# Kernel optimization log

Measured on AMD Instinct MI355X. Metric: run time of the kernel, lower is better.

## Reference

```python
import jax, jax.numpy as jnp
import numpy as np

IN_CH = 128
OUT_CH = 128
INPUT_LEN = 512
KERNEL = 8
STRIDE = 1
OUT_LEN = (INPUT_LEN - KERNEL) // STRIDE + 1  # 505
BATCH = 64


def setup_inputs() -> dict:
    key = jax.random.key(0)
    kx, kw, kb = jax.random.split(key, 3)
    x = jax.random.normal(kx, (BATCH, IN_CH, INPUT_LEN), dtype=jnp.float32)
    weight = jax.random.normal(kw, (OUT_LEN, OUT_CH, IN_CH, KERNEL), dtype=jnp.float32)
    bias = jax.random.normal(kb, (OUT_CH, OUT_LEN), dtype=jnp.float32)
    return {"x": x, "weight": weight, "bias": bias}


def reference(x, weight, bias):
    # unfold: gather sliding windows -> [b, i, l_out, k]
    idx = jnp.arange(OUT_LEN)[:, None] * STRIDE + jnp.arange(KERNEL)[None, :]  # [l, k]
    x_unf = x[:, :, idx]  # [b, i, l, k]
    # per-position independent GEMM: 'blik,loik->bol' with x permuted to bilk
    out = jnp.einsum('bilk,loik->bol', x_unf, weight)
    out = out + bias[None, :, :]
    return out
```

## Files before the change

### kernel.cpp

```cpp
#include <hip/hip_runtime.h>
#include <hip/hip_bf16.h>

#define BATCH 64
#define IN_CH 128
#define ILEN  512
#define OLEN  505
#define OCH   128
#define KDIM  1024
#define BK    64
#define NCHK  16
#define NWG   OLEN

typedef float  f32x4  __attribute__((ext_vector_type(4)));
typedef short  bf16x8 __attribute__((ext_vector_type(8)));
typedef unsigned short u16x8 __attribute__((ext_vector_type(8)));
typedef u16x8 u16x8a __attribute__((aligned(4)));

__device__ __forceinline__ unsigned short f2bf(float f) {
  union { __hip_bfloat16 h; unsigned short s; } u;
  u.h = __float2bfloat16(f);
  return u.s;
}

__global__ __launch_bounds__(256) void lc1d_cvt(const float* __restrict__ x,
                                                unsigned short* __restrict__ xbe,
                                                unsigned short* __restrict__ xbo) {
  const int gid = blockIdx.x * 256 + threadIdx.x;
  const int row = gid >> 6;
  const int t8  = (gid & 63) << 3;
  const float* src = x + (size_t)row * ILEN + t8;
  const f32x4 v0 = *reinterpret_cast<const f32x4*>(src);
  const f32x4 v1 = *reinterpret_cast<const f32x4*>(src + 4);
  const float e8 = (t8 + 8 < ILEN) ? src[8] : 0.f;
  u16x8 e, o;
#pragma unroll
  for (int j = 0; j < 4; ++j) { e[j] = f2bf(v0[j]); e[4 + j] = f2bf(v1[j]); }
  o[0] = e[1]; o[1] = e[2]; o[2] = e[3];
  o[3] = e[4]; o[4] = e[5]; o[5] = e[6]; o[6] = e[7];
  o[7] = f2bf(e8);
  *reinterpret_cast<u16x8*>(xbe + (size_t)row * ILEN + t8) = e;
  *reinterpret_cast<u16x8*>(xbo + (size_t)row * ILEN + t8) = o;
}

template <bool USE_TMP>
__global__ __launch_bounds__(256, 2) void lc1d_main(
    const unsigned short* __restrict__ xbe, const unsigned short* __restrict__ xbo,
    const float* __restrict__ w, const float* __restrict__ bias,
    float* __restrict__ outp) {
  const int orig = blockIdx.x;
  const int xcd = orig & 7, idx = orig >> 3;
  const int q = NWG / 8, rm = NWG % 8;
  const int l = (xcd < rm ? xcd * (q + 1) : rm * (q + 1) + (xcd - rm) * q) + idx;

  const int tid  = threadIdx.x;
  const int lane = tid & 63;
  const int wn   = tid >> 6;
  const int r    = lane & 15;
  const int h    = lane >> 4;

  __shared__ float Bs[2][2][BK * 64];
  __shared__ short As[2][BATCH * 64];

  f32x4 acc[2][4];
#pragma unroll
  for (int oh = 0; oh < 2; ++oh)
#pragma unroll
    for (int m = 0; m < 4; ++m) acc[oh][m] = (f32x4){0.f, 0.f, 0.f, 0.f};

  const float* __restrict__ wl = w + (size_t)l * (OCH * KDIM);
  const unsigned short* __restrict__ xw =
      ((l & 1) ? xbo : xbe) + (size_t)(l & ~1);

  const int so  = tid >> 4;
  const int sc  = tid & 15;
  const int ssw = ((so & 7) << 1) | ((so >> 3) & 1);
  const int bA = tid & 63;
  const int iw = tid >> 6;

  u16x8 va, vb;
  auto loadA2 = [&](int kc) {
    const int i0 = kc * 8 + iw * 2;
    const unsigned short* p = xw + (size_t)(bA * IN_CH + i0) * ILEN;
    va = *reinterpret_cast<const u16x8a*>(p);
    vb = *reinterpret_cast<const u16x8a*>(p + ILEN);
  };
  auto writeA2 = [&](int buf) {
    const int c0 = iw * 2;
    *reinterpret_cast<u16x8*>(&As[buf][bA * 64 + ((c0 ^ (bA & 7)) << 3)]) = va;
    *reinterpret_cast<u16x8*>(&As[buf][bA * 64 + (((c0 + 1) ^ (bA & 7)) << 3)]) = vb;
  };
  auto stageB = [&](int buf, int kc, int oh) {
    const float* wo = wl + (size_t)oh * 64 * KDIM;
#pragma unroll
    for (int it = 0; it < 4; ++it) {
      const int ob = it * 16 + so;
      const float* src = wo + (size_t)ob * KDIM + kc * BK + (sc ^ ssw) * 4;
      __builtin_amdgcn_global_load_lds(
          (const __attribute__((address_space(1))) void*)src,
          (__attribute__((address_space(3))) void*)&Bs[buf][oh][ob * 64 + sc * 4],
          16, 0, 0);
    }
  };

  const int rsw = ((r & 7) << 1) | ((r >> 3) & 1);
  auto compute = [&](int cur, int oh) {
    const int ob = wn * 16 + r;
#pragma unroll
    for (int ks = 0; ks < 2; ++ks) {
      const int c0 = ks * 8 + h * 2;
      const f32x4 blo = *reinterpret_cast<const f32x4*>(
          &Bs[cur][oh][ob * 64 + ((c0) ^ rsw) * 4]);
      const f32x4 bhi = *reinterpret_cast<const f32x4*>(
          &Bs[cur][oh][ob * 64 + ((c0 + 1) ^ rsw) * 4]);
      bf16x8 bfr;
#pragma unroll
      for (int j = 0; j < 4; ++j) {
        bfr[j]     = (short)f2bf(blo[j]);
        bfr[4 + j] = (short)f2bf(bhi[j]);
      }
#pragma unroll
      for (int mt = 0; mt < 4; ++mt) {
        const int b = mt * 16 + r;
        const bf16x8 afr = *reinterpret_cast<const bf16x8*>(
            &As[cur][b * 64 + (((ks * 4 + h) ^ (r & 7)) << 3)]);
        acc[oh][mt] =
            __builtin_amdgcn_mfma_f32_16x16x32_bf16(afr, bfr, acc[oh][mt], 0, 0, 0);
      }
    }
  };

  loadA2(0);
  stageB(0, 0, 0);
  stageB(0, 0, 1);
  writeA2(0);
  asm volatile("s_waitcnt vmcnt(0) lgkmcnt(0)" ::: "memory");
  __builtin_amdgcn_sched_barrier(0);
  __builtin_amdgcn_s_barrier();
  __builtin_amdgcn_sched_barrier(0);

  for (int kc = 0; kc < NCHK; ++kc) {
    const int cur = kc & 1, nxt = cur ^ 1;
    if (kc + 1 < NCHK) {
      loadA2(kc + 1);
      stageB(nxt, kc + 1, 0);
      stageB(nxt, kc + 1, 1);
    }
    __builtin_amdgcn_sched_barrier(0);
    compute(cur, 0);
    compute(cur, 1);
    if (kc + 1 < NCHK) {
      writeA2(nxt);
      asm volatile("s_waitcnt vmcnt(0) lgkmcnt(0)" ::: "memory");
      __builtin_amdgcn_sched_barrier(0);
      __builtin_amdgcn_s_barrier();
      __builtin_amdgcn_sched_barrier(0);
    }
  }

#pragma unroll
  for (int oh = 0; oh < 2; ++oh) {
    const int og = oh * 64 + wn * 16 + r;
    if (USE_TMP) {
      float* t = outp + (size_t)l * (BATCH * OCH) + og;
#pragma unroll
      for (int mt = 0; mt < 4; ++mt)
#pragma unroll
        for (int j = 0; j < 4; ++j) {
          const int b = mt * 16 + h * 4 + j;
          t[(size_t)b * OCH] = acc[oh][mt][j];
        }
    } else {
      const float bv = bias[og * OLEN + l];
#pragma unroll
      for (int mt = 0; mt < 4; ++mt)
#pragma unroll
        for (int j = 0; j < 4; ++j) {
          const int b = mt * 16 + h * 4 + j;
          outp[(size_t)b * (OCH * OLEN) + (size_t)og * OLEN + l] = acc[oh][mt][j] + bv;
        }
    }
  }
}

__global__ __launch_bounds__(256) void lc1d_tr(const float* __restrict__ tmp,
                                               const float* __restrict__ bias,
                                               float* __restrict__ out) {
  const int l0  = blockIdx.x * 64;
  const int bo0 = blockIdx.y * 64;
  const int tid = threadIdx.x;
  __shared__ float t[64][65];

  const int boj = tid & 63, lq = tid >> 6;
#pragma unroll
  for (int rr = 0; rr < 16; ++rr) {
    const int li = rr * 4 + lq;
    const int l  = l0 + li;
    if (l < OLEN) t[li][boj] = tmp[(size_t)l * (BATCH * OCH) + bo0 + boj];
  }
  __syncthreads();
  const int lj = tid & 63, bq = tid >> 6;
  const int l  = l0 + lj;
#pragma unroll
  for (int rr = 0; rr < 16; ++rr) {
    const int bl = rr * 4 + bq;
    const int bo = bo0 + bl;
    if (l < OLEN) {
      const int oc = bo & (OCH - 1);
      out[(size_t)bo * OLEN + l] = t[lj][bl] + bias[oc * OLEN + l];
    }
  }
}

__global__ void lc1d_naive(const float* __restrict__ x, const float* __restrict__ w,
                           const float* __restrict__ bias, float* __restrict__ out) {
  const int l = blockIdx.x, o = blockIdx.y, b = threadIdx.x;
  const float* wr = w + ((size_t)l * OCH + o) * KDIM;
  const float* xr = x + (size_t)b * (IN_CH * ILEN);
  float s = 0.f;
  for (int i = 0; i < IN_CH; ++i)
#pragma unroll
    for (int k = 0; k < 8; ++k) s += xr[i * ILEN + l + k] * wr[i * 8 + k];
  out[((size_t)b * OCH + o) * OLEN + l] = s + bias[o * OLEN + l];
}

extern "C" void kernel_launch(void* const* d_in, const int* in_sizes, int n_in,
                              void* d_out, int out_size, void* d_ws, size_t ws_size,
                              hipStream_t stream) {
  const float* x    = (const float*)d_in[0];
  const float* w    = (const float*)d_in[1];
  const float* bias = (const float*)d_in[2];
  float* out        = (float*)d_out;

  const size_t TMPB = (size_t)OLEN * BATCH * OCH * sizeof(float);
  const size_t off1 = (TMPB + 255) & ~(size_t)255;
  const size_t XBB  = (size_t)BATCH * IN_CH * ILEN * sizeof(short);
  const size_t need = off1 + 2 * XBB;

  if (ws_size >= need) {
    float* tmp = (float*)d_ws;
    unsigned short* xbe = (unsigned short*)((char*)d_ws + off1);
    unsigned short* xbo = (unsigned short*)((char*)d_ws + off1 + XBB);
    lc1d_cvt<<<dim3(2048), 256, 0, stream>>>(x, xbe, xbo);
    lc1d_main<true><<<dim3(NWG), 256, 0, stream>>>(xbe, xbo, w, bias, tmp);
    lc1d_tr<<<dim3(8, 128), 256, 0, stream>>>(tmp, bias, out);
  } else {
    lc1d_naive<<<dim3(OLEN, OCH), BATCH, 0, stream>>>(x, w, bias, out);
  }
}
```

Before: 105.8 us.

## Load A fragments directly from global into registers, drop A LDS staging

Removes the shared-memory staging buffer for the activation (A) operand. Each lane now loads its MFMA A fragments straight from global memory into double-buffered registers, prefetching the next chunk while the current one computes. The wait now keeps the 8 in-flight A loads outstanding (vmcnt(8)) so only the B LDS loads must finish before the barrier. This cuts LDS writes and reads for A and frees LDS, at the cost of more registers, a fully unrolled k-loop, and less-coalesced global loads that each wave issues redundantly.

```diff
diff --git a/kernel.cpp b/kernel.cpp
--- a/kernel.cpp
+++ b/kernel.cpp
@@ -59,7 +59,6 @@
   const int h    = lane >> 4;
 
   __shared__ float Bs[2][2][BK * 64];
-  __shared__ short As[2][BATCH * 64];
 
   f32x4 acc[2][4];
 #pragma unroll
@@ -74,21 +73,7 @@
   const int so  = tid >> 4;
   const int sc  = tid & 15;
   const int ssw = ((so & 7) << 1) | ((so >> 3) & 1);
-  const int bA = tid & 63;
-  const int iw = tid >> 6;
-
-  u16x8 va, vb;
-  auto loadA2 = [&](int kc) {
-    const int i0 = kc * 8 + iw * 2;
-    const unsigned short* p = xw + (size_t)(bA * IN_CH + i0) * ILEN;
-    va = *reinterpret_cast<const u16x8a*>(p);
-    vb = *reinterpret_cast<const u16x8a*>(p + ILEN);
-  };
-  auto writeA2 = [&](int buf) {
-    const int c0 = iw * 2;
-    *reinterpret_cast<u16x8*>(&As[buf][bA * 64 + ((c0 ^ (bA & 7)) << 3)]) = va;
-    *reinterpret_cast<u16x8*>(&As[buf][bA * 64 + (((c0 + 1) ^ (bA & 7)) << 3)]) = vb;
-  };
+
   auto stageB = [&](int buf, int kc, int oh) {
     const float* wo = wl + (size_t)oh * 64 * KDIM;
 #pragma unroll
@@ -102,8 +87,22 @@
     }
   };
 
+  u16x8 paE[4][2], paO[4][2];
+  const unsigned short* __restrict__ xbase =
+      xw + (size_t)(r * IN_CH + h) * ILEN;
+
+  auto prefA = [&](u16x8 (&pa)[4][2], int kc) {
+#pragma unroll
+    for (int mt = 0; mt < 4; ++mt) {
+      const unsigned short* p =
+          xbase + (size_t)(mt * 16 * IN_CH + kc * 8) * ILEN;
+      pa[mt][0] = *reinterpret_cast<const u16x8a*>(p);
+      pa[mt][1] = *reinterpret_cast<const u16x8a*>(p + 4 * ILEN);
+    }
+  };
+
   const int rsw = ((r & 7) << 1) | ((r >> 3) & 1);
-  auto compute = [&](int cur, int oh) {
+  auto compute = [&](int cur, u16x8 (&pa)[4][2], int oh) {
     const int ob = wn * 16 + r;
 #pragma unroll
     for (int ks = 0; ks < 2; ++ks) {
@@ -120,37 +119,34 @@
       }
 #pragma unroll
       for (int mt = 0; mt < 4; ++mt) {
-        const int b = mt * 16 + r;
-        const bf16x8 afr = *reinterpret_cast<const bf16x8*>(
-            &As[cur][b * 64 + (((ks * 4 + h) ^ (r & 7)) << 3)]);
+        const bf16x8 afr = (bf16x8)pa[mt][ks];
         acc[oh][mt] =
             __builtin_amdgcn_mfma_f32_16x16x32_bf16(afr, bfr, acc[oh][mt], 0, 0, 0);
       }
     }
   };
 
-  loadA2(0);
   stageB(0, 0, 0);
   stageB(0, 0, 1);
-  writeA2(0);
-  asm volatile("s_waitcnt vmcnt(0) lgkmcnt(0)" ::: "memory");
+  prefA(paE, 0);
+  asm volatile("s_waitcnt vmcnt(8)" ::: "memory");
   __builtin_amdgcn_sched_barrier(0);
   __builtin_amdgcn_s_barrier();
   __builtin_amdgcn_sched_barrier(0);
 
+#pragma unroll
   for (int kc = 0; kc < NCHK; ++kc) {
     const int cur = kc & 1, nxt = cur ^ 1;
     if (kc + 1 < NCHK) {
-      loadA2(kc + 1);
       stageB(nxt, kc + 1, 0);
       stageB(nxt, kc + 1, 1);
+      if ((kc & 1) == 0) prefA(paO, kc + 1); else prefA(paE, kc + 1);
     }
     __builtin_amdgcn_sched_barrier(0);
-    compute(cur, 0);
-    compute(cur, 1);
+    if ((kc & 1) == 0) { compute(cur, paE, 0); compute(cur, paE, 1); }
+    else               { compute(cur, paO, 0); compute(cur, paO, 1); }
     if (kc + 1 < NCHK) {
-      writeA2(nxt);
-      asm volatile("s_waitcnt vmcnt(0) lgkmcnt(0)" ::: "memory");
+      asm volatile("s_waitcnt vmcnt(8) lgkmcnt(0)" ::: "memory");
       __builtin_amdgcn_sched_barrier(0);
       __builtin_amdgcn_s_barrier();
       __builtin_amdgcn_sched_barrier(0);
```

Measured after the change: 149.7 us. 41.5% more time.

## Stage weights through registers as bf16 with two-chunk-ahead prefetch

Applied to the files above, without the earlier changes.

Weights are now loaded from global memory into registers two K-chunks ahead, converted to bf16 once, and written to LDS as bf16. The old path used direct global-to-LDS fp32 loads and converted inside compute. This halves LDS footprint for B and removes per-wave redundant conversions, enabling 3 workgroups per CU via launch bounds. The cost is higher register pressure (two sets of 8 f32x4 prefetch buffers) and a fully unrolled K loop, which may cause spills under the tighter occupancy bound.

```diff
diff --git a/kernel.cpp b/kernel.cpp
--- a/kernel.cpp
+++ b/kernel.cpp
@@ -43,7 +43,7 @@
 }
 
 template <bool USE_TMP>
-__global__ __launch_bounds__(256, 2) void lc1d_main(
+__global__ __launch_bounds__(256, 3) void lc1d_main(
     const unsigned short* __restrict__ xbe, const unsigned short* __restrict__ xbo,
     const float* __restrict__ w, const float* __restrict__ bias,
     float* __restrict__ outp) {
@@ -58,8 +58,8 @@
   const int r    = lane & 15;
   const int h    = lane >> 4;
 
-  __shared__ float Bs[2][2][BK * 64];
-  __shared__ short As[2][BATCH * 64];
+  __shared__ short Bs[2][OCH * BK];
+  __shared__ short As[2][BATCH * BK];
 
   f32x4 acc[2][4];
 #pragma unroll
@@ -71,86 +71,88 @@
   const unsigned short* __restrict__ xw =
       ((l & 1) ? xbo : xbe) + (size_t)(l & ~1);
 
-  const int so  = tid >> 4;
-  const int sc  = tid & 15;
-  const int ssw = ((so & 7) << 1) | ((so >> 3) & 1);
   const int bA = tid & 63;
   const int iw = tid >> 6;
-
   u16x8 va, vb;
-  auto loadA2 = [&](int kc) {
-    const int i0 = kc * 8 + iw * 2;
-    const unsigned short* p = xw + (size_t)(bA * IN_CH + i0) * ILEN;
+  auto loadA = [&](int kc) {
+    const unsigned short* p = xw + (size_t)(bA * IN_CH + kc * 8 + iw * 2) * ILEN;
     va = *reinterpret_cast<const u16x8a*>(p);
     vb = *reinterpret_cast<const u16x8a*>(p + ILEN);
   };
-  auto writeA2 = [&](int buf) {
+  auto writeA = [&](int buf) {
     const int c0 = iw * 2;
     *reinterpret_cast<u16x8*>(&As[buf][bA * 64 + ((c0 ^ (bA & 7)) << 3)]) = va;
     *reinterpret_cast<u16x8*>(&As[buf][bA * 64 + (((c0 + 1) ^ (bA & 7)) << 3)]) = vb;
   };
-  auto stageB = [&](int buf, int kc, int oh) {
-    const float* wo = wl + (size_t)oh * 64 * KDIM;
+
+  const int sc3 = tid & 7;
+  const int soB = tid >> 3;
+  f32x4 bb0[4][2], bb1[4][2];
+  auto loadB = [&](f32x4 (&bb)[4][2], int kc) {
 #pragma unroll
     for (int it = 0; it < 4; ++it) {
-      const int ob = it * 16 + so;
-      const float* src = wo + (size_t)ob * KDIM + kc * BK + (sc ^ ssw) * 4;
-      __builtin_amdgcn_global_load_lds(
-          (const __attribute__((address_space(1))) void*)src,
-          (__attribute__((address_space(3))) void*)&Bs[buf][oh][ob * 64 + sc * 4],
-          16, 0, 0);
-    }
-  };
-
-  const int rsw = ((r & 7) << 1) | ((r >> 3) & 1);
+      const int o = it * 32 + soB;
+      const float* src = wl + (size_t)o * KDIM + kc * BK + sc3 * 8;
+      bb[it][0] = *reinterpret_cast<const f32x4*>(src);
+      bb[it][1] = *reinterpret_cast<const f32x4*>(src + 4);
+    }
+  };
+  auto writeB = [&](const f32x4 (&bb)[4][2], int buf) {
+#pragma unroll
+    for (int it = 0; it < 4; ++it) {
+      const int o = it * 32 + soB;
+      u16x8 v;
+#pragma unroll
+      for (int j = 0; j < 4; ++j) {
+        v[j]     = f2bf(bb[it][0][j]);
+        v[4 + j] = f2bf(bb[it][1][j]);
+      }
+      *reinterpret_cast<u16x8*>(&Bs[buf][o * 64 + ((sc3 ^ (o & 7)) << 3)]) = v;
+    }
+  };
+
   auto compute = [&](int cur, int oh) {
-    const int ob = wn * 16 + r;
+    const int ob = oh * 64 + wn * 16 + r;
 #pragma unroll
     for (int ks = 0; ks < 2; ++ks) {
-      const int c0 = ks * 8 + h * 2;
-      const f32x4 blo = *reinterpret_cast<const f32x4*>(
-          &Bs[cur][oh][ob * 64 + ((c0) ^ rsw) * 4]);
-      const f32x4 bhi = *reinterpret_cast<const f32x4*>(
-          &Bs[cur][oh][ob * 64 + ((c0 + 1) ^ rsw) * 4]);
-      bf16x8 bfr;
-#pragma unroll
-      for (int j = 0; j < 4; ++j) {
-        bfr[j]     = (short)f2bf(blo[j]);
-        bfr[4 + j] = (short)f2bf(bhi[j]);
-      }
+      const int c = ks * 4 + h;
+      const bf16x8 bfr = *reinterpret_cast<const bf16x8*>(
+          &Bs[cur][ob * 64 + ((c ^ (ob & 7)) << 3)]);
 #pragma unroll
       for (int mt = 0; mt < 4; ++mt) {
         const int b = mt * 16 + r;
         const bf16x8 afr = *reinterpret_cast<const bf16x8*>(
-            &As[cur][b * 64 + (((ks * 4 + h) ^ (r & 7)) << 3)]);
+            &As[cur][b * 64 + ((c ^ (b & 7)) << 3)]);
         acc[oh][mt] =
             __builtin_amdgcn_mfma_f32_16x16x32_bf16(afr, bfr, acc[oh][mt], 0, 0, 0);
       }
     }
   };
 
-  loadA2(0);
-  stageB(0, 0, 0);
-  stageB(0, 0, 1);
-  writeA2(0);
-  asm volatile("s_waitcnt vmcnt(0) lgkmcnt(0)" ::: "memory");
+  loadA(0);
+  loadB(bb0, 0);
+  loadB(bb1, 1);
+  writeA(0);
+  writeB(bb0, 0);
+  asm volatile("s_waitcnt lgkmcnt(0)" ::: "memory");
   __builtin_amdgcn_sched_barrier(0);
   __builtin_amdgcn_s_barrier();
   __builtin_amdgcn_sched_barrier(0);
 
+#pragma unroll
   for (int kc = 0; kc < NCHK; ++kc) {
     const int cur = kc & 1, nxt = cur ^ 1;
-    if (kc + 1 < NCHK) {
-      loadA2(kc + 1);
-      stageB(nxt, kc + 1, 0);
-      stageB(nxt, kc + 1, 1);
+    if (kc + 1 < NCHK) loadA(kc + 1);
+    if (kc + 2 < NCHK) {
+      if ((kc & 1) == 0) loadB(bb0, kc + 2); else loadB(bb1, kc + 2);
     }
     __builtin_amdgcn_sched_barrier(0);
     compute(cur, 0);
     compute(cur, 1);
     if (kc + 1 < NCHK) {
-      writeA2(nxt);
-      asm volatile("s_waitcnt vmcnt(0) lgkmcnt(0)" ::: "memory");
+      writeA(nxt);
+      if ((kc & 1) == 0) writeB(bb1, nxt); else writeB(bb0, nxt);
+      asm volatile("s_waitcnt lgkmcnt(0)" ::: "memory");
       __builtin_amdgcn_sched_barrier(0);
       __builtin_amdgcn_s_barrier();
       __builtin_amdgcn_sched_barrier(0);
```

After: 113.1 us. 1.07x slower.

## Split output-channel halves across workgroups, prefetch A two chunks ahead, store bf16 temp

Applied to the files above, without the earlier changes.

Launches one workgroup per (position, output-channel half), which doubles the grid and halves LDS and accumulator use so three workgroups can fit per CU. A-operand global loads now run two chunks ahead using alternating register sets and a partial vmcnt wait, which is meant to hide global latency behind compute. The intermediate buffer is written as bf16 instead of fp32 to cut temp write and read traffic, at the cost of extra rounding error in the output. Each workgroup now reads the shared input tile separately, so input reads are duplicated.

```diff
diff --git a/kernel.cpp b/kernel.cpp
--- a/kernel.cpp
+++ b/kernel.cpp
@@ -9,17 +9,23 @@
 #define KDIM  1024
 #define BK    64
 #define NCHK  16
-#define NWG   OLEN
+#define NWG   (OLEN * 2)
 
 typedef float  f32x4  __attribute__((ext_vector_type(4)));
 typedef short  bf16x8 __attribute__((ext_vector_type(8)));
 typedef unsigned short u16x8 __attribute__((ext_vector_type(8)));
 typedef u16x8 u16x8a __attribute__((aligned(4)));
 
-__device__ __forceinline__ unsigned short f2bf(float f) {
+__device__ __forceinline__ unsigned short f2bfu(float f) {
   union { __hip_bfloat16 h; unsigned short s; } u;
   u.h = __float2bfloat16(f);
   return u.s;
+}
+__device__ __forceinline__ short f2bf(float f) { return (short)f2bfu(f); }
+__device__ __forceinline__ float bf2f(unsigned short s) {
+  union { unsigned int u; float f; } u;
+  u.u = ((unsigned int)s) << 16;
+  return u.f;
 }
 
 __global__ __launch_bounds__(256) void lc1d_cvt(const float* __restrict__ x,
@@ -34,23 +40,25 @@
   const float e8 = (t8 + 8 < ILEN) ? src[8] : 0.f;
   u16x8 e, o;
 #pragma unroll
-  for (int j = 0; j < 4; ++j) { e[j] = f2bf(v0[j]); e[4 + j] = f2bf(v1[j]); }
+  for (int j = 0; j < 4; ++j) { e[j] = f2bfu(v0[j]); e[4 + j] = f2bfu(v1[j]); }
   o[0] = e[1]; o[1] = e[2]; o[2] = e[3];
   o[3] = e[4]; o[4] = e[5]; o[5] = e[6]; o[6] = e[7];
-  o[7] = f2bf(e8);
+  o[7] = f2bfu(e8);
   *reinterpret_cast<u16x8*>(xbe + (size_t)row * ILEN + t8) = e;
   *reinterpret_cast<u16x8*>(xbo + (size_t)row * ILEN + t8) = o;
 }
 
 template <bool USE_TMP>
-__global__ __launch_bounds__(256, 2) void lc1d_main(
+__global__ __launch_bounds__(256, 3) void lc1d_main(
     const unsigned short* __restrict__ xbe, const unsigned short* __restrict__ xbo,
     const float* __restrict__ w, const float* __restrict__ bias,
-    float* __restrict__ outp) {
+    void* __restrict__ outp) {
   const int orig = blockIdx.x;
   const int xcd = orig & 7, idx = orig >> 3;
   const int q = NWG / 8, rm = NWG % 8;
-  const int l = (xcd < rm ? xcd * (q + 1) : rm * (q + 1) + (xcd - rm) * q) + idx;
+  const int wg = (xcd < rm ? xcd * (q + 1) : rm * (q + 1) + (xcd - rm) * q) + idx;
+  const int l  = wg >> 1;
+  const int oh = wg & 1;
 
   const int tid  = threadIdx.x;
   const int lane = tid & 63;
@@ -58,131 +66,132 @@
   const int r    = lane & 15;
   const int h    = lane >> 4;
 
-  __shared__ float Bs[2][2][BK * 64];
+  __shared__ float Bs[2][BK * 64];
   __shared__ short As[2][BATCH * 64];
 
-  f32x4 acc[2][4];
-#pragma unroll
-  for (int oh = 0; oh < 2; ++oh)
-#pragma unroll
-    for (int m = 0; m < 4; ++m) acc[oh][m] = (f32x4){0.f, 0.f, 0.f, 0.f};
-
-  const float* __restrict__ wl = w + (size_t)l * (OCH * KDIM);
+  f32x4 acc[4];
+#pragma unroll
+  for (int m = 0; m < 4; ++m) acc[m] = (f32x4){0.f, 0.f, 0.f, 0.f};
+
+  const float* __restrict__ wo =
+      w + (size_t)l * (OCH * KDIM) + (size_t)oh * 64 * KDIM;
   const unsigned short* __restrict__ xw =
       ((l & 1) ? xbo : xbe) + (size_t)(l & ~1);
 
   const int so  = tid >> 4;
   const int sc  = tid & 15;
   const int ssw = ((so & 7) << 1) | ((so >> 3) & 1);
-  const int bA = tid & 63;
-  const int iw = tid >> 6;
-
-  u16x8 va, vb;
-  auto loadA2 = [&](int kc) {
-    const int i0 = kc * 8 + iw * 2;
-    const unsigned short* p = xw + (size_t)(bA * IN_CH + i0) * ILEN;
-    va = *reinterpret_cast<const u16x8a*>(p);
-    vb = *reinterpret_cast<const u16x8a*>(p + ILEN);
-  };
-  auto writeA2 = [&](int buf) {
-    const int c0 = iw * 2;
-    *reinterpret_cast<u16x8*>(&As[buf][bA * 64 + ((c0 ^ (bA & 7)) << 3)]) = va;
-    *reinterpret_cast<u16x8*>(&As[buf][bA * 64 + (((c0 + 1) ^ (bA & 7)) << 3)]) = vb;
-  };
-  auto stageB = [&](int buf, int kc, int oh) {
-    const float* wo = wl + (size_t)oh * 64 * KDIM;
+  auto stageB = [&](int buf, int kc) {
 #pragma unroll
     for (int it = 0; it < 4; ++it) {
       const int ob = it * 16 + so;
       const float* src = wo + (size_t)ob * KDIM + kc * BK + (sc ^ ssw) * 4;
       __builtin_amdgcn_global_load_lds(
           (const __attribute__((address_space(1))) void*)src,
-          (__attribute__((address_space(3))) void*)&Bs[buf][oh][ob * 64 + sc * 4],
+          (__attribute__((address_space(3))) void*)&Bs[buf][ob * 64 + sc * 4],
           16, 0, 0);
     }
   };
 
+  const int bA = tid & 63;
+  const int iw = tid >> 6;
+  u16x8 vaE, vbE, vaO, vbO;
+  auto loadA2 = [&](u16x8& va, u16x8& vb, int kc) {
+    const unsigned short* p = xw + (size_t)(bA * IN_CH + kc * 8 + iw * 2) * ILEN;
+    va = *reinterpret_cast<const u16x8a*>(p);
+    vb = *reinterpret_cast<const u16x8a*>(p + ILEN);
+  };
+  auto writeA2 = [&](const u16x8& va, const u16x8& vb, int buf) {
+    const int c0 = iw * 2;
+    *reinterpret_cast<u16x8*>(&As[buf][bA * 64 + ((c0 ^ (bA & 7)) << 3)]) = va;
+    *reinterpret_cast<u16x8*>(&As[buf][bA * 64 + (((c0 + 1) ^ (bA & 7)) << 3)]) = vb;
+  };
+
   const int rsw = ((r & 7) << 1) | ((r >> 3) & 1);
-  auto compute = [&](int cur, int oh) {
+  auto compute = [&](int cur) {
     const int ob = wn * 16 + r;
 #pragma unroll
     for (int ks = 0; ks < 2; ++ks) {
       const int c0 = ks * 8 + h * 2;
-      const f32x4 blo = *reinterpret_cast<const f32x4*>(
-          &Bs[cur][oh][ob * 64 + ((c0) ^ rsw) * 4]);
-      const f32x4 bhi = *reinterpret_cast<const f32x4*>(
-          &Bs[cur][oh][ob * 64 + ((c0 + 1) ^ rsw) * 4]);
-      bf16x8 bfr;
-#pragma unroll
-      for (int j = 0; j < 4; ++j) {
-        bfr[j]     = (short)f2bf(blo[j]);
-        bfr[4 + j] = (short)f2bf(bhi[j]);
-      }
+      bf16x8 af[4];
 #pragma unroll
       for (int mt = 0; mt < 4; ++mt) {
         const int b = mt * 16 + r;
-        const bf16x8 afr = *reinterpret_cast<const bf16x8*>(
-            &As[cur][b * 64 + (((ks * 4 + h) ^ (r & 7)) << 3)]);
-        acc[oh][mt] =
-            __builtin_amdgcn_mfma_f32_16x16x32_bf16(afr, bfr, acc[oh][mt], 0, 0, 0);
-      }
-    }
-  };
-
-  loadA2(0);
-  stageB(0, 0, 0);
-  stageB(0, 0, 1);
-  writeA2(0);
-  asm volatile("s_waitcnt vmcnt(0) lgkmcnt(0)" ::: "memory");
+        af[mt] = *reinterpret_cast<const bf16x8*>(
+            &As[cur][b * 64 + (((ks * 4 + h) ^ (b & 7)) << 3)]);
+      }
+      const f32x4 blo = *reinterpret_cast<const f32x4*>(
+          &Bs[cur][ob * 64 + ((c0) ^ rsw) * 4]);
+      const f32x4 bhi = *reinterpret_cast<const f32x4*>(
+          &Bs[cur][ob * 64 + ((c0 + 1) ^ rsw) * 4]);
+      bf16x8 bfr;
+#pragma unroll
+      for (int j = 0; j < 4; ++j) {
+        bfr[j]     = f2bf(blo[j]);
+        bfr[4 + j] = f2bf(bhi[j]);
+      }
+#pragma unroll
+      for (int mt = 0; mt < 4; ++mt)
+        acc[mt] = __builtin_amdgcn_mfma_f32_16x16x32_bf16(af[mt], bfr, acc[mt], 0, 0, 0);
+    }
+  };
+
+  loadA2(vaE, vbE, 0);
+  stageB(0, 0);
+  writeA2(vaE, vbE, 0);
+  loadA2(vaO, vbO, 1);
+  asm volatile("s_waitcnt vmcnt(2) lgkmcnt(0)" ::: "memory");
   __builtin_amdgcn_sched_barrier(0);
   __builtin_amdgcn_s_barrier();
   __builtin_amdgcn_sched_barrier(0);
 
-  for (int kc = 0; kc < NCHK; ++kc) {
-    const int cur = kc & 1, nxt = cur ^ 1;
+  auto step = [&](int kc, u16x8& aW0, u16x8& aW1, u16x8& aL0, u16x8& aL1) {
+    if (kc + 1 < NCHK) stageB((kc + 1) & 1, kc + 1);
+    if (kc + 2 < NCHK) loadA2(aL0, aL1, kc + 2);
+    __builtin_amdgcn_sched_barrier(0);
+    compute(kc & 1);
     if (kc + 1 < NCHK) {
-      loadA2(kc + 1);
-      stageB(nxt, kc + 1, 0);
-      stageB(nxt, kc + 1, 1);
-    }
-    __builtin_amdgcn_sched_barrier(0);
-    compute(cur, 0);
-    compute(cur, 1);
-    if (kc + 1 < NCHK) {
-      writeA2(nxt);
-      asm volatile("s_waitcnt vmcnt(0) lgkmcnt(0)" ::: "memory");
+      writeA2(aW0, aW1, (kc + 1) & 1);
+      if (kc + 2 < NCHK) {
+        asm volatile("s_waitcnt vmcnt(2) lgkmcnt(0)" ::: "memory");
+      } else {
+        asm volatile("s_waitcnt vmcnt(0) lgkmcnt(0)" ::: "memory");
+      }
       __builtin_amdgcn_sched_barrier(0);
       __builtin_amdgcn_s_barrier();
       __builtin_amdgcn_sched_barrier(0);
     }
-  }
-
-#pragma unroll
-  for (int oh = 0; oh < 2; ++oh) {
-    const int og = oh * 64 + wn * 16 + r;
-    if (USE_TMP) {
-      float* t = outp + (size_t)l * (BATCH * OCH) + og;
-#pragma unroll
-      for (int mt = 0; mt < 4; ++mt)
-#pragma unroll
-        for (int j = 0; j < 4; ++j) {
-          const int b = mt * 16 + h * 4 + j;
-          t[(size_t)b * OCH] = acc[oh][mt][j];
-        }
-    } else {
-      const float bv = bias[og * OLEN + l];
-#pragma unroll
-      for (int mt = 0; mt < 4; ++mt)
-#pragma unroll
-        for (int j = 0; j < 4; ++j) {
-          const int b = mt * 16 + h * 4 + j;
-          outp[(size_t)b * (OCH * OLEN) + (size_t)og * OLEN + l] = acc[oh][mt][j] + bv;
-        }
-    }
-  }
-}
-
-__global__ __launch_bounds__(256) void lc1d_tr(const float* __restrict__ tmp,
+  };
+
+  for (int kc = 0; kc < NCHK; kc += 2) {
+    step(kc, vaO, vbO, vaE, vbE);
+    step(kc + 1, vaE, vbE, vaO, vbO);
+  }
+
+  const int og = oh * 64 + wn * 16 + r;
+  if (USE_TMP) {
+    unsigned short* t = (unsigned short*)outp + (size_t)l * (BATCH * OCH) + og;
+#pragma unroll
+    for (int mt = 0; mt < 4; ++mt)
+#pragma unroll
+      for (int j = 0; j < 4; ++j) {
+        const int b = mt * 16 + h * 4 + j;
+        t[(size_t)b * OCH] = f2bfu(acc[mt][j]);
+      }
+  } else {
+    const float bv = bias[og * OLEN + l];
+#pragma unroll
+    for (int mt = 0; mt < 4; ++mt)
+#pragma unroll
+      for (int j = 0; j < 4; ++j) {
+        const int b = mt * 16 + h * 4 + j;
+        ((float*)outp)[(size_t)b * (OCH * OLEN) + (size_t)og * OLEN + l] =
+            acc[mt][j] + bv;
+      }
+  }
+}
+
+__global__ __launch_bounds__(256) void lc1d_tr(const unsigned short* __restrict__ tmp,
                                                const float* __restrict__ bias,
                                                float* __restrict__ out) {
   const int l0  = blockIdx.x * 64;
@@ -195,7 +204,8 @@
   for (int rr = 0; rr < 16; ++rr) {
     const int li = rr * 4 + lq;
     const int l  = l0 + li;
-    if (l < OLEN) t[li][boj] = tmp[(size_t)l * (BATCH * OCH) + bo0 + boj];
+    if (l < OLEN)
+      t[li][boj] = bf2f(tmp[(size_t)l * (BATCH * OCH) + bo0 + boj]);
   }
   __syncthreads();
   const int lj = tid & 63, bq = tid >> 6;
@@ -231,17 +241,17 @@
   const float* bias = (const float*)d_in[2];
   float* out        = (float*)d_out;
 
-  const size_t TMPB = (size_t)OLEN * BATCH * OCH * sizeof(float);
+  const size_t TMPB = (size_t)OLEN * BATCH * OCH * sizeof(unsigned short);
   const size_t off1 = (TMPB + 255) & ~(size_t)255;
   const size_t XBB  = (size_t)BATCH * IN_CH * ILEN * sizeof(short);
   const size_t need = off1 + 2 * XBB;
 
   if (ws_size >= need) {
-    float* tmp = (float*)d_ws;
+    unsigned short* tmp = (unsigned short*)d_ws;
     unsigned short* xbe = (unsigned short*)((char*)d_ws + off1);
     unsigned short* xbo = (unsigned short*)((char*)d_ws + off1 + XBB);
     lc1d_cvt<<<dim3(2048), 256, 0, stream>>>(x, xbe, xbo);
-    lc1d_main<true><<<dim3(NWG), 256, 0, stream>>>(xbe, xbo, w, bias, tmp);
+    lc1d_main<true><<<dim3(NWG), 256, 0, stream>>>(xbe, xbo, w, bias, (void*)tmp);
     lc1d_tr<<<dim3(8, 128), 256, 0, stream>>>(tmp, bias, out);
   } else {
     lc1d_naive<<<dim3(OLEN, OCH), BATCH, 0, stream>>>(x, w, bias, out);
```

Result: slower. 123.4 us (+16.7%).
